# Kernel optimization log

Hardware: AMD Instinct MI355X
Metric: run time of the kernel (lower is better)

The kernel has to match this reference:

```python
import jax, jax.numpy as jnp
import numpy as np

HEADS = 4


def setup_inputs() -> dict:
    key = jax.random.key(0)
    ks = jax.random.split(key, 5)
    B, T, C, H, W = 2, 16, 256, 64, 64
    x = jax.random.normal(ks[0], (B, T, C, H, W), dtype=jnp.float32)
    s = 1.0 / np.sqrt(C).astype(np.float32)  # kaiming-ish init scale for 1x1 conv
    Wq = jax.random.normal(ks[1], (C, C), dtype=jnp.float32) * s
    Wk = jax.random.normal(ks[2], (C, C), dtype=jnp.float32) * s
    Wv = jax.random.normal(ks[3], (C, C), dtype=jnp.float32) * s
    Wp = jax.random.normal(ks[4], (C, C), dtype=jnp.float32) * s
    return {"x": x, "Wq": Wq, "Wk": Wk, "Wv": Wv, "Wp": Wp}


def reference(x, Wq, Wk, Wv, Wp):
    B, T, C, H, W = x.shape
    heads = HEADS
    Ch = C // heads
    scale = Ch ** (-0.5)
    # [B,T,C,H,W] -> [B*H*W, T, C]: each spatial pixel has a T x C temporal track
    xf = jnp.transpose(x, (0, 3, 4, 1, 2)).reshape(B * H * W, T, C)
    # Conv1d(C,C,1,bias=False) == channel matmul: out[n,t,d] = sum_c W[d,c] x[n,t,c]
    q = jnp.einsum('ntc,dc->ntd', xf, Wq).reshape(-1, T, heads, Ch) * scale
    k = jnp.einsum('ntc,dc->ntd', xf, Wk).reshape(-1, T, heads, Ch)
    v = jnp.einsum('ntc,dc->ntd', xf, Wv).reshape(-1, T, heads, Ch)
    k_soft = jax.nn.softmax(k, axis=1)    # softmax over time T (torch dim=-1 of [n,h,c,t])
    q_soft = jax.nn.softmax(q, axis=-1)   # softmax over head channels Ch (torch dim=-2)
    # linear attention: outer-product context then query contraction
    kv = jnp.einsum('nthc,nthd->nhcd', k_soft, v)         # [N,h,Ch,Ch]
    out = jnp.einsum('nthc,nhcd->nthd', q_soft, kv)       # [N,T,h,Ch]
    out = out.reshape(-1, T, C)
    out = jnp.einsum('ntc,dc->ntd', out, Wp)
    out = out.reshape(B, H, W, T, C)
    return jnp.transpose(out, (0, 3, 4, 1, 2))
```

## Files before the change

### kernel.cpp

```cpp
#include <hip/hip_runtime.h>
#include <hip/hip_bf16.h>

#define DI __device__ __forceinline__

typedef __attribute__((ext_vector_type(8))) short bf16x8;
typedef __attribute__((ext_vector_type(4))) float f32x4;
typedef __attribute__((ext_vector_type(4))) _Float16 f16x4;

constexpr int XPAD = 264;
constexpr float LOG2E = 1.4426950408889634f;

DI float fexp(float x) { return __builtin_amdgcn_exp2f(x * LOG2E); }
DI float frcp(float x) { return __builtin_amdgcn_rcpf(x); }

DI short f2bf(float f) {
  __hip_bfloat16 h = __float2bfloat16(f);
  union { __hip_bfloat16 h; short s; } c; c.h = h; return c.s;
}

DI unsigned pk2(float a, float b) {
  union { __hip_bfloat162 h; unsigned u; } c;
  c.h.x = __float2bfloat16(a); c.h.y = __float2bfloat16(b);
  return c.u;
}

DI short f2h(float f) {
  _Float16 h = (_Float16)f;
  union { _Float16 h; short s; } c; c.h = h; return c.s;
}

DI f16x4 pkh4(float a, float b, float c, float d) {
  auto lo = __builtin_amdgcn_cvt_pkrtz(a, b);
  auto hi = __builtin_amdgcn_cvt_pkrtz(c, d);
  union { struct { decltype(lo) l, h; } p; f16x4 v; } u;
  u.p.l = lo; u.p.h = hi;
  return u.v;
}

DI f16x4 ld4h(const short* p) {
  union { uint2 u; f16x4 v; } c;
  c.u = *(const uint2*)p;
  return c.v;
}

DI f32x4 mfma16(bf16x8 a, bf16x8 b, f32x4 c) {
  return __builtin_amdgcn_mfma_f32_16x16x32_bf16(a, b, c, 0, 0, 0);
}

DI f32x4 mfmah(f16x4 a, f16x4 b, f32x4 c) {
  return __builtin_amdgcn_mfma_f32_16x16x16f16(a, b, c, 0, 0, 0);
}

DI f32x4 fzero() { return f32x4{0.f, 0.f, 0.f, 0.f}; }

DI int xsw(int row, int e) { return row * 256 + (e ^ ((row & 7) << 3)); }

__global__ void wconv_kernel(const float* __restrict__ a, const float* __restrict__ b,
                             const float* __restrict__ c, const float* __restrict__ d,
                             short* __restrict__ o) {
  int i = blockIdx.x * 256 + threadIdx.x;
  int mat = i >> 14;
  int off = (i & 16383) * 4;
  const float* s = (mat == 0) ? a : (mat == 1) ? b : (mat == 2) ? c : d;
  const float sc = (mat == 0) ? 0.125f : 1.0f;
  float4 v = *(const float4*)(s + off);
  uint2 r; r.x = pk2(v.x * sc, v.y * sc); r.y = pk2(v.z * sc, v.w * sc);
  *(uint2*)(o + mat * 65536 + off) = r;
}

__global__ __launch_bounds__(256, 4)
void k1_kernel(const float* __restrict__ x, const short* __restrict__ wbf,
               short* __restrict__ att, short* __restrict__ qsg, int n0chunk) {
  __shared__ short SMEM[16384];
  short* Xs = SMEM;

  const int tid  = threadIdx.x;
  const int wave = tid >> 6;
  const int lane = tid & 63;
  const int g    = lane >> 4;
  const int li   = lane & 15;

  int bid = blockIdx.x;
  const int nb = gridDim.x;
  if ((nb & 7) == 0) { const int q = nb >> 3; bid = (bid & 7) * q + (bid >> 3); }

  const int n0  = n0chunk + bid * 4;
  const int b   = n0 >> 12;
  const int hw0 = n0 & 4095;
  const float* xb = x + (size_t)b * (16 * 256 * 4096) + hw0;

  {
    const int c4 = lane;
    #pragma unroll
    for (int it = 0; it < 4; ++it) {
      const int t = it * 4 + wave;
      const float* src = xb + (size_t)(t * 256 + c4 * 4) * 4096;
      float4 v0 = *(const float4*)(src);
      float4 v1 = *(const float4*)(src + 4096);
      float4 v2 = *(const float4*)(src + 8192);
      float4 v3 = *(const float4*)(src + 12288);
      uint2 s0; s0.x = pk2(v0.x, v1.x); s0.y = pk2(v2.x, v3.x);
      uint2 s1; s1.x = pk2(v0.y, v1.y); s1.y = pk2(v2.y, v3.y);
      uint2 s2; s2.x = pk2(v0.z, v1.z); s2.y = pk2(v2.z, v3.z);
      uint2 s3; s3.x = pk2(v0.w, v1.w); s3.y = pk2(v2.w, v3.w);
      *(uint2*)&Xs[xsw(0 * 16 + t, c4 * 4)] = s0;
      *(uint2*)&Xs[xsw(1 * 16 + t, c4 * 4)] = s1;
      *(uint2*)&Xs[xsw(2 * 16 + t, c4 * 4)] = s2;
      *(uint2*)&Xs[xsw(3 * 16 + t, c4 * 4)] = s3;
    }
  }
  __syncthreads();

  const short* wq = wbf;
  const short* wk = wbf + 65536;
  const short* wv = wbf + 131072;
  const size_t wrow = (size_t)(wave * 64) * 256;
  short* qsw = qsg + ((size_t)bid * 4 * 4 + wave) * 1024;

  {
    f32x4 qacc[4][4];
    #pragma unroll
    for (int p = 0; p < 4; ++p)
      #pragma unroll
      for (int nt = 0; nt < 4; ++nt) qacc[p][nt] = fzero();

    __builtin_amdgcn_s_setprio(1);
    #pragma unroll
    for (int ks = 0; ks < 8; ++ks) {
      bf16x8 qb[4];
      #pragma unroll
      for (int nt = 0; nt < 4; ++nt)
        qb[nt] = *(const bf16x8*)(wq + wrow + (size_t)(nt * 16 + li) * 256 + ks * 32 + g * 8);
      #pragma unroll
      for (int p = 0; p < 4; ++p) {
        bf16x8 af = *(const bf16x8*)&Xs[xsw(p * 16 + li, ks * 32 + g * 8)];
        #pragma unroll
        for (int nt = 0; nt < 4; ++nt)
          qacc[p][nt] = mfma16(af, qb[nt], qacc[p][nt]);
      }
    }
    __builtin_amdgcn_s_setprio(0);

    #pragma unroll
    for (int p = 0; p < 4; ++p) {
      short* qsp = qsw + p * 4096;
      #pragma unroll
      for (int r = 0; r < 4; ++r) {
        float e0 = fexp(qacc[p][0][r]);
        float e1 = fexp(qacc[p][1][r]);
        float e2 = fexp(qacc[p][2][r]);
        float e3 = fexp(qacc[p][3][r]);
        float s = e0 + e1 + e2 + e3;
        s += __shfl_xor(s, 1); s += __shfl_xor(s, 2);
        s += __shfl_xor(s, 4); s += __shfl_xor(s, 8);
        const float inv = frcp(s);
        const int t = g * 4 + r;
        short* dst = qsp + t * 64 + li;
        dst[0]  = f2h(e0 * inv);
        dst[16] = f2h(e1 * inv);
        dst[32] = f2h(e2 * inv);
        dst[48] = f2h(e3 * inv);
      }
    }
  }

  f16x4 akf[4][4];
  {
    f32x4 kacc[4][4];
    #pragma unroll
    for (int p = 0; p < 4; ++p)
      #pragma unroll
      for (int nt = 0; nt < 4; ++nt) kacc[p][nt] = fzero();

    __builtin_amdgcn_s_setprio(1);
    #pragma unroll
    for (int ks = 0; ks < 8; ++ks) {
      bf16x8 kb[4];
      #pragma unroll
      for (int nt = 0; nt < 4; ++nt)
        kb[nt] = *(const bf16x8*)(wk + wrow + (size_t)(nt * 16 + li) * 256 + ks * 32 + g * 8);
      #pragma unroll
      for (int p = 0; p < 4; ++p) {
        bf16x8 af = *(const bf16x8*)&Xs[xsw(p * 16 + li, ks * 32 + g * 8)];
        #pragma unroll
        for (int nt = 0; nt < 4; ++nt)
          kacc[p][nt] = mfma16(af, kb[nt], kacc[p][nt]);
      }
    }
    __builtin_amdgcn_s_setprio(0);

    #pragma unroll
    for (int p = 0; p < 4; ++p)
      #pragma unroll
      for (int nt = 0; nt < 4; ++nt) {
        float e0 = fexp(kacc[p][nt][0]);
        float e1 = fexp(kacc[p][nt][1]);
        float e2 = fexp(kacc[p][nt][2]);
        float e3 = fexp(kacc[p][nt][3]);
        float s = e0 + e1 + e2 + e3;
        s += __shfl_xor(s, 16);
        s += __shfl_xor(s, 32);
        const float inv = frcp(s);
        akf[p][nt] = pkh4(e0 * inv, e1 * inv, e2 * inv, e3 * inv);
      }
  }

  f16x4 bvf[4][4];
  #pragma unroll
  for (int h = 0; h < 2; ++h) {
    f32x4 vacc[4][2];
    #pragma unroll
    for (int p = 0; p < 4; ++p)
      #pragma unroll
      for (int n2 = 0; n2 < 2; ++n2) vacc[p][n2] = fzero();

    __builtin_amdgcn_s_setprio(1);
    #pragma unroll
    for (int ks = 0; ks < 8; ++ks) {
      bf16x8 vb[2];
      #pragma unroll
      for (int n2 = 0; n2 < 2; ++n2)
        vb[n2] = *(const bf16x8*)(wv + wrow + (size_t)((h * 2 + n2) * 16 + li) * 256 + ks * 32 + g * 8);
      #pragma unroll
      for (int p = 0; p < 4; ++p) {
        bf16x8 af = *(const bf16x8*)&Xs[xsw(p * 16 + li, ks * 32 + g * 8)];
        #pragma unroll
        for (int n2 = 0; n2 < 2; ++n2)
          vacc[p][n2] = mfma16(af, vb[n2], vacc[p][n2]);
      }
    }
    __builtin_amdgcn_s_setprio(0);

    #pragma unroll
    for (int p = 0; p < 4; ++p)
      #pragma unroll
      for (int n2 = 0; n2 < 2; ++n2)
        bvf[p][h * 2 + n2] = pkh4(vacc[p][n2][0], vacc[p][n2][1],
                                  vacc[p][n2][2], vacc[p][n2][3]);
  }

  asm volatile("s_waitcnt vmcnt(0)" ::: "memory");

  #pragma unroll
  for (int p = 0; p < 4; ++p) {
    const short* qsp = qsw + p * 4096;
    f32x4 oacc[4];
    #pragma unroll
    for (int nt = 0; nt < 4; ++nt) oacc[nt] = fzero();

    #pragma unroll
    for (int cq = 0; cq < 4; ++cq) {
      f32x4 kva[4];
      #pragma unroll
      for (int nt = 0; nt < 4; ++nt)
        kva[nt] = mfmah(akf[p][cq], bvf[p][nt], fzero());
      f16x4 aq = ld4h(qsp + li * 64 + cq * 16 + g * 4);
      #pragma unroll
      for (int nt = 0; nt < 4; ++nt) {
        f16x4 kb16 = pkh4(kva[nt][0], kva[nt][1], kva[nt][2], kva[nt][3]);
        oacc[nt] = mfmah(aq, kb16, oacc[nt]);
      }
    }

    const size_t arow = ((size_t)bid * 4 + p) * 16;
    #pragma unroll
    for (int nt = 0; nt < 4; ++nt)
      #pragma unroll
      for (int r = 0; r < 4; ++r)
        att[(arow + g * 4 + r) * 256 + wave * 64 + nt * 16 + li] = f2bf(oacc[nt][r]);
  }
}

__global__ __launch_bounds__(256, 2)
void k2_kernel(const short* __restrict__ att, const short* __restrict__ wpb,
               float* __restrict__ out, int n0chunk) {
  __shared__ short A[128 * XPAD];
  const int tid = threadIdx.x;
  const int wave = tid >> 6, lane = tid & 63, g = lane >> 4, li = lane & 15;
  const int pb = blockIdx.x >> 1;
  const int t0 = (blockIdx.x & 1) * 8;
  const int n0 = n0chunk + pb * 16;
  const int b = n0 >> 12, hw0 = n0 & 4095;

  for (int idx = tid; idx < 128 * 32; idx += 256) {
    const int row = idx >> 5, seg = idx & 31;
    const int p = row & 15, tl = row >> 4;
    const short* src = att + ((size_t)((pb * 16 + p) * 16 + t0 + tl)) * 256 + seg * 8;
    *(int4*)&A[row * XPAD + seg * 8] = *(const int4*)src;
  }
  __syncthreads();

  f32x4 acc[8][4];
  #pragma unroll
  for (int mt = 0; mt < 8; ++mt)
    #pragma unroll
    for (int n4 = 0; n4 < 4; ++n4) acc[mt][n4] = fzero();

  #pragma unroll
  for (int ks = 0; ks < 8; ++ks) {
    bf16x8 bf[4];
    #pragma unroll
    for (int n4 = 0; n4 < 4; ++n4)
      bf[n4] = *(const bf16x8*)(wpb + (size_t)((wave * 4 + n4) * 16 + li) * 256 + ks * 32 + g * 8);
    #pragma unroll
    for (int mt = 0; mt < 8; ++mt) {
      bf16x8 af = *(const bf16x8*)&A[(mt * 16 + li) * XPAD + ks * 32 + g * 8];
      #pragma unroll
      for (int n4 = 0; n4 < 4; ++n4) acc[mt][n4] = mfma16(af, bf[n4], acc[mt][n4]);
    }
  }

  float* ob = out + (size_t)b * (16 * 256 * 4096) + hw0;
  #pragma unroll
  for (int mt = 0; mt < 8; ++mt)
    #pragma unroll
    for (int n4 = 0; n4 < 4; ++n4) {
      const int t = t0 + mt;
      const int c = (wave * 4 + n4) * 16 + li;
      float4 v;
      v.x = acc[mt][n4][0]; v.y = acc[mt][n4][1];
      v.z = acc[mt][n4][2]; v.w = acc[mt][n4][3];
      *(float4*)(ob + (size_t)(t * 256 + c) * 4096 + g * 4) = v;
    }
}

extern "C" void kernel_launch(void* const* d_in, const int* in_sizes, int n_in,
                              void* d_out, int out_size, void* d_ws, size_t ws_size,
                              hipStream_t stream) {
  const float* x  = (const float*)d_in[0];
  const float* Wq = (const float*)d_in[1];
  const float* Wk = (const float*)d_in[2];
  const float* Wv = (const float*)d_in[3];
  const float* Wp = (const float*)d_in[4];
  float* out = (float*)d_out;

  short* wbf = (short*)d_ws;
  short* att = wbf + 4 * 65536;

  wconv_kernel<<<256, 256, 0, stream>>>(Wq, Wk, Wv, Wp, wbf);

  const size_t wsAvail = (ws_size > 524288) ? (ws_size - 524288) : 0;
  const size_t perPix = 16 * 256 * 2;
  int chunk = 16;
  while (chunk < 8192 && (size_t)(chunk * 2) * perPix <= wsAvail) chunk <<= 1;

  short* qsg = att + (size_t)chunk * 4096;

  for (int n0 = 0; n0 < 8192; n0 += chunk) {
    k1_kernel<<<chunk / 4, 256, 0, stream>>>(x, wbf, att, qsg, n0);
    k2_kernel<<<(chunk / 16) * 2, 256, 0, stream>>>(att, wbf + 3 * 65536, out, n0);
  }
}
```

Before: 242.4 us.

## Fuse output projection into attention kernel via LDS staging

Removes the separate k2 projection kernel. The attention output is now written as bf16 into swizzled shared memory and multiplied by Wp inside k1, with fp32 results stored directly to the output tensor. This avoids writing and re-reading the intermediate attention buffer in global memory and drops one launch per chunk. The cost is extra work and register pressure in k1, and output stores now cover only 4 pixels per block, which are narrower and less coalesced than k2's 16-pixel tiles.

```diff
diff --git a/kernel.cpp b/kernel.cpp
--- a/kernel.cpp
+++ b/kernel.cpp
@@ -7,7 +7,6 @@
 typedef __attribute__((ext_vector_type(4))) float f32x4;
 typedef __attribute__((ext_vector_type(4))) _Float16 f16x4;
 
-constexpr int XPAD = 264;
 constexpr float LOG2E = 1.4426950408889634f;
 
 DI float fexp(float x) { return __builtin_amdgcn_exp2f(x * LOG2E); }
@@ -70,9 +69,10 @@
 
 __global__ __launch_bounds__(256, 4)
 void k1_kernel(const float* __restrict__ x, const short* __restrict__ wbf,
-               short* __restrict__ att, short* __restrict__ qsg, int n0chunk) {
+               float* __restrict__ out, short* __restrict__ qsg, int n0chunk) {
   __shared__ short SMEM[16384];
   short* Xs = SMEM;
+  short* att_lds = SMEM;
 
   const int tid  = threadIdx.x;
   const int wave = tid >> 6;
@@ -240,6 +240,7 @@
   }
 
   asm volatile("s_waitcnt vmcnt(0)" ::: "memory");
+  __syncthreads();
 
   #pragma unroll
   for (int p = 0; p < 4; ++p) {
@@ -262,66 +263,55 @@
       }
     }
 
-    const size_t arow = ((size_t)bid * 4 + p) * 16;
     #pragma unroll
     for (int nt = 0; nt < 4; ++nt)
       #pragma unroll
-      for (int r = 0; r < 4; ++r)
-        att[(arow + g * 4 + r) * 256 + wave * 64 + nt * 16 + li] = f2bf(oacc[nt][r]);
-  }
-}
-
-__global__ __launch_bounds__(256, 2)
-void k2_kernel(const short* __restrict__ att, const short* __restrict__ wpb,
-               float* __restrict__ out, int n0chunk) {
-  __shared__ short A[128 * XPAD];
-  const int tid = threadIdx.x;
-  const int wave = tid >> 6, lane = tid & 63, g = lane >> 4, li = lane & 15;
-  const int pb = blockIdx.x >> 1;
-  const int t0 = (blockIdx.x & 1) * 8;
-  const int n0 = n0chunk + pb * 16;
-  const int b = n0 >> 12, hw0 = n0 & 4095;
-
-  for (int idx = tid; idx < 128 * 32; idx += 256) {
-    const int row = idx >> 5, seg = idx & 31;
-    const int p = row & 15, tl = row >> 4;
-    const short* src = att + ((size_t)((pb * 16 + p) * 16 + t0 + tl)) * 256 + seg * 8;
-    *(int4*)&A[row * XPAD + seg * 8] = *(const int4*)src;
-  }
+      for (int r = 0; r < 4; ++r) {
+        const int row = (g * 4 + r) * 4 + p;
+        att_lds[xsw(row, wave * 64 + nt * 16 + li)] = f2bf(oacc[nt][r]);
+      }
+  }
+
   __syncthreads();
 
-  f32x4 acc[8][4];
-  #pragma unroll
-  for (int mt = 0; mt < 8; ++mt)
-    #pragma unroll
-    for (int n4 = 0; n4 < 4; ++n4) acc[mt][n4] = fzero();
-
-  #pragma unroll
-  for (int ks = 0; ks < 8; ++ks) {
-    bf16x8 bf[4];
-    #pragma unroll
-    for (int n4 = 0; n4 < 4; ++n4)
-      bf[n4] = *(const bf16x8*)(wpb + (size_t)((wave * 4 + n4) * 16 + li) * 256 + ks * 32 + g * 8);
-    #pragma unroll
-    for (int mt = 0; mt < 8; ++mt) {
-      bf16x8 af = *(const bf16x8*)&A[(mt * 16 + li) * XPAD + ks * 32 + g * 8];
-      #pragma unroll
-      for (int n4 = 0; n4 < 4; ++n4) acc[mt][n4] = mfma16(af, bf[n4], acc[mt][n4]);
-    }
-  }
-
-  float* ob = out + (size_t)b * (16 * 256 * 4096) + hw0;
-  #pragma unroll
-  for (int mt = 0; mt < 8; ++mt)
-    #pragma unroll
-    for (int n4 = 0; n4 < 4; ++n4) {
-      const int t = t0 + mt;
-      const int c = (wave * 4 + n4) * 16 + li;
-      float4 v;
-      v.x = acc[mt][n4][0]; v.y = acc[mt][n4][1];
-      v.z = acc[mt][n4][2]; v.w = acc[mt][n4][3];
-      *(float4*)(ob + (size_t)(t * 256 + c) * 4096 + g * 4) = v;
-    }
+  {
+    const short* wp = wbf + 3 * 65536;
+    f32x4 pacc[4][4];
+    #pragma unroll
+    for (int mt = 0; mt < 4; ++mt)
+      #pragma unroll
+      for (int n4 = 0; n4 < 4; ++n4) pacc[mt][n4] = fzero();
+
+    __builtin_amdgcn_s_setprio(1);
+    #pragma unroll
+    for (int ks = 0; ks < 8; ++ks) {
+      bf16x8 bw[4];
+      #pragma unroll
+      for (int n4 = 0; n4 < 4; ++n4)
+        bw[n4] = *(const bf16x8*)(wp + (size_t)((wave * 4 + n4) * 16 + li) * 256 + ks * 32 + g * 8);
+      #pragma unroll
+      for (int mt = 0; mt < 4; ++mt) {
+        bf16x8 af = *(const bf16x8*)&att_lds[xsw(mt * 16 + li, ks * 32 + g * 8)];
+        #pragma unroll
+        for (int n4 = 0; n4 < 4; ++n4)
+          pacc[mt][n4] = mfma16(af, bw[n4], pacc[mt][n4]);
+      }
+    }
+    __builtin_amdgcn_s_setprio(0);
+
+    float* ob = out + (size_t)b * (16 * 256 * 4096) + hw0;
+    #pragma unroll
+    for (int mt = 0; mt < 4; ++mt)
+      #pragma unroll
+      for (int n4 = 0; n4 < 4; ++n4) {
+        const int t = mt * 4 + g;
+        const int c = (wave * 4 + n4) * 16 + li;
+        float4 v;
+        v.x = pacc[mt][n4][0]; v.y = pacc[mt][n4][1];
+        v.z = pacc[mt][n4][2]; v.w = pacc[mt][n4][3];
+        *(float4*)(ob + (size_t)(t * 256 + c) * 4096) = v;
+      }
+  }
 }
 
 extern "C" void kernel_launch(void* const* d_in, const int* in_sizes, int n_in,
@@ -335,19 +325,16 @@
   float* out = (float*)d_out;
 
   short* wbf = (short*)d_ws;
-  short* att = wbf + 4 * 65536;
+  short* qsg = wbf + 4 * 65536;
 
   wconv_kernel<<<256, 256, 0, stream>>>(Wq, Wk, Wv, Wp, wbf);
 
   const size_t wsAvail = (ws_size > 524288) ? (ws_size - 524288) : 0;
   const size_t perPix = 16 * 256 * 2;
   int chunk = 16;
-  while (chunk < 8192 && (size_t)(chunk * 2) * perPix <= wsAvail) chunk <<= 1;
-
-  short* qsg = att + (size_t)chunk * 4096;
+  while (chunk < 8192 && (size_t)(chunk * 1) * perPix <= wsAvail) chunk <<= 1;
 
   for (int n0 = 0; n0 < 8192; n0 += chunk) {
-    k1_kernel<<<chunk / 4, 256, 0, stream>>>(x, wbf, att, qsg, n0);
-    k2_kernel<<<(chunk / 16) * 2, 256, 0, stream>>>(att, wbf + 3 * 65536, out, n0);
-  }
-}
+    k1_kernel<<<chunk / 4, 256, 0, stream>>>(x, wbf, out, qsg, n0);
+  }
+}
```

Result: slower. 293.1 us (+20.9%).
